# Kernel tuning notes

Hardware: AMD Instinct MI355X
Metric: run time of the kernel (lower is better)

The kernel has to match this reference:

```python
import jax, jax.numpy as jnp
import numpy as np

B = 256      # number of graphs (args.batch_size)
NPG = 1000   # nodes per graph (args.num_node)
C = 64       # in_channels
DEG = 16     # avg degree
K = 500      # ceil(ratio * NPG), ratio = 0.5
EPS = 1e-8


def setup_inputs() -> dict:
    key = jax.random.key(0)
    k1, k2, k3, k4, k5 = jax.random.split(key, 5)
    N = B * NPG
    epg = NPG * DEG  # edges per graph
    x = jax.random.normal(k1, (N, C), jnp.float32)
    src = jax.random.randint(k2, (B, epg), 0, NPG)
    dst = jax.random.randint(k3, (B, epg), 0, NPG)
    off = (jnp.arange(B, dtype=jnp.int32) * NPG)[:, None]
    edge_index = jnp.stack([(src + off).reshape(-1), (dst + off).reshape(-1)]).astype(jnp.int32)
    edge_attr = jax.random.uniform(k4, (B * epg,), jnp.float32)
    batch = jnp.repeat(jnp.arange(B, dtype=jnp.int32), NPG)
    W = jax.random.normal(k5, (C, C), jnp.float32) * (1.0 / np.sqrt(C))
    b = jnp.zeros((C,), jnp.float32)
    return {"istraining": 1, "x": x, "edge_index": edge_index, "edge_attr": edge_attr,
            "batch": batch, "W": W, "b": b}


def _gcn_conv(x, edge_index, W, b):
    # PyG GCNConv: x' = D^{-1/2} (A + I) D^{-1/2} X W + b, unit edge weights.
    N = x.shape[0]
    sl = jnp.arange(N, dtype=edge_index.dtype)
    src = jnp.concatenate([edge_index[0], sl])  # message source j
    dst = jnp.concatenate([edge_index[1], sl])  # aggregation target i
    deg = jnp.zeros((N,), x.dtype).at[dst].add(1.0)
    dinv = jnp.where(deg > 0, jax.lax.rsqrt(jnp.maximum(deg, 1.0)), 0.0)
    norm = dinv[src] * dinv[dst]          # [E+N]
    h = x @ W                              # [N, C]
    msg = h[src] * norm[:, None]           # gather + scale (dominant traffic)
    out = jax.ops.segment_sum(msg, dst, num_segments=N) + b
    return out


def _node_score(x):
    # compute_node_score: cosine similarity of each node to its graph centroid
    # (community prototype), plus KL(softmax(score) || uniform) per graph.
    xb = x.reshape(B, NPG, C)
    cen = xb.mean(axis=1, keepdims=True)                       # [B,1,C]
    num = jnp.sum(xb * cen, axis=-1)                           # [B,NPG]
    den = jnp.linalg.norm(xb, axis=-1) * jnp.linalg.norm(cen, axis=-1) + EPS
    score = num / den                                          # [B,NPG]
    logp = jax.nn.log_softmax(score, axis=1)
    kl = jnp.sum(jnp.exp(logp) * (logp + jnp.log(jnp.float32(NPG))), axis=1)  # [B]
    indices_ = jnp.argsort(-score, axis=1)                     # [B,NPG]
    return score, kl, indices_


def reference(istraining, x, edge_index, edge_attr, batch, W, b):
    N = x.shape[0]
    x = _gcn_conv(x, edge_index, W, b)
    score, kl_all_batch, indices_ = _node_score(x)
    # per-graph top-k (fixed k since every graph has NPG nodes)
    _, idx = jax.lax.top_k(score, K)                           # [B,K]
    perm = ((jnp.arange(B, dtype=idx.dtype) * NPG)[:, None] + idx).reshape(-1)  # [B*K]
    score_flat = score.reshape(-1)
    x_new = x[perm] * jnp.tanh(score_flat[perm])[:, None]
    batch_new = batch[perm]
    # filter_adj: keep edges with both endpoints retained, re-index to new ids.
    mapping = jnp.full((N,), -1, dtype=jnp.int32).at[perm].set(
        jnp.arange(perm.shape[0], dtype=jnp.int32))
    new_ei = mapping[edge_index]                               # [2,E], -1 = dropped
    edge_mask = jnp.logical_and(new_ei[0] >= 0, new_ei[1] >= 0)
    edge_attr_new = jnp.where(edge_mask, edge_attr, 0.0)
    return (x_new, new_ei, edge_attr_new, edge_mask, batch_new, perm, kl_all_batch, indices_)
```

## Files before the change

kernel.cpp:

```cpp
#include <hip/hip_runtime.h>
#include <math.h>

#define NPG 1000
#define KTOP 500
#define C 64
#define EPG 16000

__device__ __forceinline__ float readlane_f(float v, int l) {
    return __uint_as_float(__builtin_amdgcn_readlane(__float_as_uint(v), (unsigned)l));
}
__device__ __forceinline__ int readlane_i(int v, int l) {
    return (int)__builtin_amdgcn_readlane((unsigned)v, (unsigned)l);
}

__global__ __launch_bounds__(256) void build_graph_k(const int* __restrict__ ei, int E,
                                                     int* __restrict__ deg,
                                                     float* __restrict__ dinv,
                                                     int* __restrict__ off,
                                                     int* __restrict__ csr,
                                                     float* __restrict__ wcsr) {
    int g = blockIdx.x, t = threadIdx.x;
    __shared__ int cnt[NPG];
    __shared__ int soff[NPG];
    __shared__ float sdinv[NPG];
    __shared__ unsigned short lcsr[EPG];
    __shared__ int red[256];
    const int gbase = g * NPG;
    const int ebase = g * EPG;
    const int* __restrict__ srcp = ei + ebase;
    const int* __restrict__ dstp = ei + E + ebase;

    for (int i = t; i < NPG; i += 256) cnt[i] = 0;
    __syncthreads();
    for (int i = t; i < EPG; i += 256) atomicAdd(&cnt[dstp[i] - gbase], 1);
    __syncthreads();
    int base = t * 4;
    int v0 = 0, v1 = 0, v2 = 0, v3 = 0;
    if (base + 0 < NPG) v0 = cnt[base + 0];
    if (base + 1 < NPG) v1 = cnt[base + 1];
    if (base + 2 < NPG) v2 = cnt[base + 2];
    if (base + 3 < NPG) v3 = cnt[base + 3];
    int s = v0 + v1 + v2 + v3;
    red[t] = s;
    __syncthreads();
    for (int o = 1; o < 256; o <<= 1) {
        int xx = (t >= o) ? red[t - o] : 0;
        __syncthreads();
        red[t] += xx;
        __syncthreads();
    }
    int p = red[t] - s;
    if (base + 0 < NPG) { soff[base + 0] = p; p += v0; }
    if (base + 1 < NPG) { soff[base + 1] = p; p += v1; }
    if (base + 2 < NPG) { soff[base + 2] = p; p += v2; }
    if (base + 3 < NPG) { soff[base + 3] = p; p += v3; }
    __syncthreads();
    for (int i = t; i < NPG; i += 256) {
        int d = cnt[i];
        deg[gbase + i] = d;
        float dv = 1.0f / sqrtf((float)(d + 1));
        dinv[gbase + i] = dv;
        sdinv[i] = dv;
        off[gbase + i] = ebase + soff[i];
    }
    __syncthreads();
    for (int i = t; i < NPG; i += 256) cnt[i] = soff[i];
    __syncthreads();
    for (int i = t; i < EPG; i += 256) {
        int d = dstp[i] - gbase;
        int pos = atomicAdd(&cnt[d], 1);
        lcsr[pos] = (unsigned short)(srcp[i] - gbase);
    }
    __syncthreads();
    int4* co = (int4*)(csr + ebase);
    float4* wo = (float4*)(wcsr + ebase);
    for (int i = t; i < EPG / 4; i += 256) {
        int l0 = lcsr[i * 4 + 0], l1 = lcsr[i * 4 + 1];
        int l2 = lcsr[i * 4 + 2], l3 = lcsr[i * 4 + 3];
        int4 v;
        v.x = gbase + l0; v.y = gbase + l1; v.z = gbase + l2; v.w = gbase + l3;
        co[i] = v;
        float4 w;
        w.x = sdinv[l0]; w.y = sdinv[l1]; w.z = sdinv[l2]; w.w = sdinv[l3];
        wo[i] = w;
    }
}

__global__ __launch_bounds__(256) void gemm_k(const float* __restrict__ x,
                                              const float* __restrict__ W,
                                              float* __restrict__ h, int N) {
    __shared__ float sW[C * C];
    int t = threadIdx.x;
    for (int i = t; i < C * C / 4; i += 256) ((float4*)sW)[i] = ((const float4*)W)[i];
    __syncthreads();
    int r0 = blockIdx.x * 512 + t;
    int r1 = r0 + 256;
    if (r0 >= N) return;
    bool has1 = (r1 < N);
    const float4* x0 = (const float4*)(x + (size_t)r0 * C);
    const float4* x1 = (const float4*)(x + (size_t)(has1 ? r1 : r0) * C);
    float acc0[C], acc1[C];
#pragma unroll
    for (int i = 0; i < C; ++i) { acc0[i] = 0.f; acc1[i] = 0.f; }
    float4 a0 = x0[0], a1 = x1[0];
    for (int k4 = 0; k4 < 16; ++k4) {
        float4 b0, b1;
        if (k4 < 15) { b0 = x0[k4 + 1]; b1 = x1[k4 + 1]; }
        const float4* wr = (const float4*)(sW + k4 * 4 * C);
        const float* a0f = (const float*)&a0;
        const float* a1f = (const float*)&a1;
#pragma unroll
        for (int c4 = 0; c4 < 16; ++c4) {
            float4 w[4];
            w[0] = wr[c4]; w[1] = wr[16 + c4]; w[2] = wr[32 + c4]; w[3] = wr[48 + c4];
            const float* wf = (const float*)w;
#pragma unroll
            for (int j = 0; j < 4; ++j) {
                float s0 = acc0[c4 * 4 + j], s1 = acc1[c4 * 4 + j];
#pragma unroll
                for (int kk = 0; kk < 4; ++kk) {
                    float wv = wf[kk * 4 + j];
                    s0 = fmaf(a0f[kk], wv, s0);
                    s1 = fmaf(a1f[kk], wv, s1);
                }
                acc0[c4 * 4 + j] = s0; acc1[c4 * 4 + j] = s1;
            }
        }
        a0 = b0; a1 = b1;
    }
    float4* h0 = (float4*)(h + (size_t)r0 * C);
#pragma unroll
    for (int q = 0; q < 16; ++q) h0[q] = ((float4*)acc0)[q];
    if (has1) {
        float4* h1 = (float4*)(h + (size_t)r1 * C);
#pragma unroll
        for (int q = 0; q < 16; ++q) h1[q] = ((float4*)acc1)[q];
    }
}

__global__ __launch_bounds__(256) void gather_k(const int* __restrict__ csr,
                                                const float* __restrict__ wcsr,
                                                const int* __restrict__ off,
                                                const int* __restrict__ deg,
                                                const float* __restrict__ h,
                                                const float* __restrict__ dinv,
                                                const float* __restrict__ bias,
                                                float* __restrict__ out2, int N, int B) {
    int b = blockIdx.x;
    int wave = threadIdx.x >> 6;
    int lane = threadIdx.x & 63;
    int node;
    if ((B & 7) == 0) {
        int xcd = b & 7, slot = b >> 3;
        int gpx = B >> 3;
        int g = xcd * gpx + slot / (NPG / 4);
        int blkin = slot % (NPG / 4);
        node = g * NPG + blkin * 4 + wave;
    } else {
        node = b * 4 + wave;
    }
    if (node >= N) return;
    int o0 = off[node], dg = deg[node];
    float di = dinv[node];
    float hv = h[(size_t)node * C + lane];
    int sv = 0; float wv = 0.f;
    if (lane < dg) { sv = csr[o0 + lane]; wv = wcsr[o0 + lane]; }
    float acc = 0.f;
    int jmax = dg < 64 ? dg : 64;
    int j = 0;
    for (; j + 4 <= jmax; j += 4) {
        int   s0 = readlane_i(sv, j + 0); float w0 = readlane_f(wv, j + 0);
        int   s1 = readlane_i(sv, j + 1); float w1 = readlane_f(wv, j + 1);
        int   s2 = readlane_i(sv, j + 2); float w2 = readlane_f(wv, j + 2);
        int   s3 = readlane_i(sv, j + 3); float w3 = readlane_f(wv, j + 3);
        float h0 = h[(size_t)s0 * C + lane];
        float h1 = h[(size_t)s1 * C + lane];
        float h2 = h[(size_t)s2 * C + lane];
        float h3 = h[(size_t)s3 * C + lane];
        acc = fmaf(h0, w0, acc);
        acc = fmaf(h1, w1, acc);
        acc = fmaf(h2, w2, acc);
        acc = fmaf(h3, w3, acc);
    }
    for (; j < jmax; ++j) {
        int s = readlane_i(sv, j); float w = readlane_f(wv, j);
        acc = fmaf(h[(size_t)s * C + lane], w, acc);
    }
    for (; j < dg; ++j) {
        int s = csr[o0 + j];
        acc = fmaf(h[(size_t)s * C + lane], dinv[s], acc);
    }
    out2[(size_t)node * C + lane] = bias[lane] + di * acc + di * di * hv;
}

__global__ void centroid_part_k(const float* __restrict__ out2, float* __restrict__ pcen) {
    int blk = blockIdx.x;
    int g = blk >> 2, p = blk & 3;
    int t = threadIdx.x;
    int c = t & 63, q = t >> 6;
    const float* base = out2 + (size_t)g * NPG * C;
    int n0 = p * 250, n1 = n0 + 250;
    float acc = 0.f;
    for (int n = n0 + q; n < n1; n += 4) acc += base[(size_t)n * C + c];
    __shared__ float red[256];
    red[t] = acc;
    __syncthreads();
    if (t < 64) pcen[(size_t)blk * C + t] = red[t] + red[64 + t] + red[128 + t] + red[192 + t];
}

__global__ void cen_fin_k(const float* __restrict__ pcen, float* __restrict__ cen,
                          float* __restrict__ cnorm) {
    int g = blockIdx.x, c = threadIdx.x;
    float s = pcen[(size_t)(g * 4 + 0) * C + c] + pcen[(size_t)(g * 4 + 1) * C + c]
            + pcen[(size_t)(g * 4 + 2) * C + c] + pcen[(size_t)(g * 4 + 3) * C + c];
    float m = s / 1000.0f;
    cen[g * C + c] = m;
    float v = m * m;
    for (int o = 32; o > 0; o >>= 1) v += __shfl_down(v, o, 64);
    if (c == 0) cnorm[g] = sqrtf(v);
}

__global__ void score_k(const float* __restrict__ out2, const float* __restrict__ cen,
                        const float* __restrict__ cnorm, float* __restrict__ score, int N) {
    int i = blockIdx.x * 256 + threadIdx.x;
    if (i < N) {
        int g = i / NPG;
        const float4* xr = (const float4*)(out2 + (size_t)i * C);
        const float4* cr = (const float4*)(cen + g * C);
        float num = 0.f, sq = 0.f;
#pragma unroll
        for (int q = 0; q < 16; ++q) {
            float4 a = xr[q], b = cr[q];
            num += a.x * b.x + a.y * b.y + a.z * b.z + a.w * b.w;
            sq  += a.x * a.x + a.y * a.y + a.z * a.z + a.w * a.w;
        }
        float den = sqrtf(sq) * cnorm[g] + 1e-8f;
        score[i] = num / den;
    }
}

__global__ void softmax_kl_k(const float* __restrict__ score, float* __restrict__ o_kl) {
    int g = blockIdx.x, t = threadIdx.x;
    __shared__ float ss[NPG];
    __shared__ float red[256];
    const float4* s4 = (const float4*)(score + (size_t)g * NPG);
    for (int i = t; i < NPG / 4; i += 256) ((float4*)ss)[i] = s4[i];
    __syncthreads();
    float mx = -INFINITY;
    for (int i = t; i < NPG; i += 256) mx = fmaxf(mx, ss[i]);
    red[t] = mx;
    __syncthreads();
    for (int w = 128; w > 0; w >>= 1) { if (t < w) red[t] = fmaxf(red[t], red[t + w]); __syncthreads(); }
    mx = red[0];
    __syncthreads();
    float se = 0.f;
    for (int i = t; i < NPG; i += 256) se += expf(ss[i] - mx);
    red[t] = se;
    __syncthreads();
    for (int w = 128; w > 0; w >>= 1) { if (t < w) red[t] += red[t + w]; __syncthreads(); }
    float lse = logf(red[0]);
    __syncthreads();
    float kl = 0.f;
    const float ln_npg = 6.9077552790f;
    for (int i = t; i < NPG; i += 256) {
        float lp = ss[i] - mx - lse;
        kl += expf(lp) * (lp + ln_npg);
    }
    red[t] = kl;
    __syncthreads();
    for (int w = 128; w > 0; w >>= 1) { if (t < w) red[t] += red[t + w]; __syncthreads(); }
    if (t == 0) o_kl[g] = red[0];
}

__global__ void sort_k(const float* __restrict__ score, int* __restrict__ sidx,
                       float* __restrict__ o_ind) {
    __shared__ unsigned long long kk[1024];
    int g = blockIdx.x, t = threadIdx.x;
    for (int i = t; i < 1024; i += 512) {
        unsigned long long v;
        if (i < NPG) {
            unsigned u = __float_as_uint(score[(size_t)g * NPG + i]);
            u = (u & 0x80000000u) ? ~u : (u | 0x80000000u);
            v = ((unsigned long long)(~u) << 32) | (unsigned)i;
        } else {
            v = ~0ULL;
        }
        kk[i] = v;
    }
    __syncthreads();
    for (int k = 2; k <= 1024; k <<= 1) {
        for (int j = k >> 1; j > 0; j >>= 1) {
            for (int i = t; i < 1024; i += 512) {
                int ixj = i ^ j;
                if (ixj > i) {
                    unsigned long long a = kk[i], b = kk[ixj];
                    bool up = ((i & k) == 0);
                    if ((a > b) == up) { kk[i] = b; kk[ixj] = a; }
                }
            }
            __syncthreads();
        }
    }
    for (int i = t; i < NPG; i += 512) {
        int idx = (int)(kk[i] & 0xFFFFFFFFULL);
        sidx[(size_t)g * NPG + i] = idx;
        o_ind[(size_t)g * NPG + i] = (float)idx;
    }
}

__global__ void topk_k(const int* __restrict__ sidx, const float* __restrict__ score,
                       const float* __restrict__ out2, int* __restrict__ mapping,
                       float* __restrict__ o_xnew, float* __restrict__ o_batch,
                       float* __restrict__ o_perm, int BK) {
    int j = blockIdx.x * 256 + threadIdx.x;
    if (j < BK) {
        int b = j / KTOP, r = j - b * KTOP;
        int node = sidx[(size_t)b * NPG + r];
        int gn = b * NPG + node;
        mapping[gn] = j;
        o_perm[j] = (float)gn;
        o_batch[j] = (float)b;
        float tn = tanhf(score[gn]);
        const float4* src = (const float4*)(out2 + (size_t)gn * C);
        float4* dst = (float4*)(o_xnew + (size_t)j * C);
#pragma unroll
        for (int q = 0; q < 16; ++q) {
            float4 v = src[q];
            v.x *= tn; v.y *= tn; v.z *= tn; v.w *= tn;
            dst[q] = v;
        }
    }
}

__global__ void edge_out_k(const int* __restrict__ ei, const float* __restrict__ eattr,
                           const int* __restrict__ mapping, float* __restrict__ o_newei,
                           float* __restrict__ o_eattr, float* __restrict__ o_mask, int E) {
    int e4 = blockIdx.x * 256 + threadIdx.x;
    int q = E >> 2;
    if (e4 < q) {
        int4 sidx = ((const int4*)ei)[e4];
        int4 didx = ((const int4*)ei)[q + e4];
        int a0 = mapping[sidx.x], a1 = mapping[sidx.y], a2 = mapping[sidx.z], a3 = mapping[sidx.w];
        int b0 = mapping[didx.x], b1 = mapping[didx.y], b2 = mapping[didx.z], b3 = mapping[didx.w];
        float4 f0 = { (float)a0, (float)a1, (float)a2, (float)a3 };
        float4 f1 = { (float)b0, (float)b1, (float)b2, (float)b3 };
        ((float4*)o_newei)[e4] = f0;
        ((float4*)o_newei)[q + e4] = f1;
        float4 at = ((const float4*)eattr)[e4];
        float4 mk, ea;
        mk.x = (a0 >= 0 && b0 >= 0) ? 1.0f : 0.0f;
        mk.y = (a1 >= 0 && b1 >= 0) ? 1.0f : 0.0f;
        mk.z = (a2 >= 0 && b2 >= 0) ? 1.0f : 0.0f;
        mk.w = (a3 >= 0 && b3 >= 0) ? 1.0f : 0.0f;
        ea.x = mk.x != 0.0f ? at.x : 0.0f;
        ea.y = mk.y != 0.0f ? at.y : 0.0f;
        ea.z = mk.z != 0.0f ? at.z : 0.0f;
        ea.w = mk.w != 0.0f ? at.w : 0.0f;
        ((float4*)o_mask)[e4] = mk;
        ((float4*)o_eattr)[e4] = ea;
    }
}

extern "C" void kernel_launch(void* const* d_in, const int* in_sizes, int n_in,
                              void* d_out, int out_size, void* d_ws, size_t ws_size,
                              hipStream_t stream) {
    (void)n_in; (void)out_size; (void)ws_size;
    const float* x     = (const float*)d_in[1];
    const int*   ei    = (const int*)d_in[2];
    const float* eattr = (const float*)d_in[3];
    const float* W     = (const float*)d_in[5];
    const float* bias  = (const float*)d_in[6];

    const int N  = in_sizes[1] / C;
    const int E  = in_sizes[2] / 2;
    const int B  = N / NPG;
    const int BK = B * KTOP;

    char* wsp = (char*)d_ws;
    float* out2    = (float*)wsp; wsp += (size_t)N * C * 4;
    float* dinv    = (float*)wsp; wsp += (size_t)N * 4;
    float* score   = (float*)wsp; wsp += (size_t)N * 4;
    float* cen     = (float*)wsp; wsp += (size_t)B * C * 4;
    float* cnorm   = (float*)wsp; wsp += 1024;
    int*   sidx    = (int*)wsp;   wsp += (size_t)B * NPG * 4;
    int*   mapping = (int*)wsp;   wsp += (size_t)N * 4;
    int*   deg     = (int*)wsp;   wsp += (size_t)N * 4;
    int*   off     = (int*)wsp;   wsp += (size_t)N * 4;
    float* pcen    = (float*)wsp; wsp += (size_t)B * 4 * C * 4;

    float* out     = (float*)d_out;
    float* o_xnew  = out;
    float* o_newei = o_xnew + (size_t)BK * C;
    float* o_eattr = o_newei + 2 * (size_t)E;
    float* o_mask  = o_eattr + (size_t)E;
    float* o_batch = o_mask + (size_t)E;
    float* o_perm  = o_batch + (size_t)BK;
    float* o_kl    = o_perm + (size_t)BK;
    float* o_ind   = o_kl + (size_t)B;

    float* hbuf = out;
    int*   csr  = (int*)o_eattr;
    float* wcsr = o_mask;

    hipMemsetAsync(mapping, 0xFF, (size_t)N * 4, stream);

    build_graph_k<<<B, 256, 0, stream>>>(ei, E, deg, dinv, off, csr, wcsr);
    gemm_k<<<(N + 511) / 512, 256, 0, stream>>>(x, W, hbuf, N);
    gather_k<<<(N + 3) / 4, 256, 0, stream>>>(csr, wcsr, off, deg, hbuf, dinv, bias, out2, N, B);
    centroid_part_k<<<B * 4, 256, 0, stream>>>(out2, pcen);
    cen_fin_k<<<B, 64, 0, stream>>>(pcen, cen, cnorm);
    score_k<<<(N + 255) / 256, 256, 0, stream>>>(out2, cen, cnorm, score, N);
    softmax_kl_k<<<B, 256, 0, stream>>>(score, o_kl);
    sort_k<<<B, 512, 0, stream>>>(score, sidx, o_ind);
    topk_k<<<(BK + 255) / 256, 256, 0, stream>>>(sidx, score, out2, mapping,
                                                 o_xnew, o_batch, o_perm, BK);
    edge_out_k<<<(E / 4 + 255) / 256, 256, 0, stream>>>(ei, eattr, mapping,
                                                        o_newei, o_eattr, o_mask, E);
}
```

Measured before the change: 494.8 us.

## Prescale GEMM output by source dinv and drop per-edge weight array

Folds the source-side D^{-1/2} normalization into the GEMM epilogue, so h2 = dinv*xW is stored directly. The gather then only sums neighbor rows, and the per-edge weight array (wcsr) no longer has to be built, written or read, which removes one global write and one read per edge along with the readlane ops. The gather inner loop is also unrolled to 8 neighbors to put more loads in flight. The GEMM gains a dependency on dinv, and the floating-point summation order changes slightly.

Result: no change. 491.7 us (-0.6%).

```diff
diff --git a/kernel.cpp b/kernel.cpp
--- a/kernel.cpp
+++ b/kernel.cpp
@@ -17,12 +17,10 @@
                                                      int* __restrict__ deg,
                                                      float* __restrict__ dinv,
                                                      int* __restrict__ off,
-                                                     int* __restrict__ csr,
-                                                     float* __restrict__ wcsr) {
+                                                     int* __restrict__ csr) {
     int g = blockIdx.x, t = threadIdx.x;
     __shared__ int cnt[NPG];
     __shared__ int soff[NPG];
-    __shared__ float sdinv[NPG];
     __shared__ unsigned short lcsr[EPG];
     __shared__ int red[256];
     const int gbase = g * NPG;
@@ -58,9 +56,7 @@
     for (int i = t; i < NPG; i += 256) {
         int d = cnt[i];
         deg[gbase + i] = d;
-        float dv = 1.0f / sqrtf((float)(d + 1));
-        dinv[gbase + i] = dv;
-        sdinv[i] = dv;
+        dinv[gbase + i] = 1.0f / sqrtf((float)(d + 1));
         off[gbase + i] = ebase + soff[i];
     }
     __syncthreads();
@@ -73,22 +69,20 @@
     }
     __syncthreads();
     int4* co = (int4*)(csr + ebase);
-    float4* wo = (float4*)(wcsr + ebase);
     for (int i = t; i < EPG / 4; i += 256) {
-        int l0 = lcsr[i * 4 + 0], l1 = lcsr[i * 4 + 1];
-        int l2 = lcsr[i * 4 + 2], l3 = lcsr[i * 4 + 3];
         int4 v;
-        v.x = gbase + l0; v.y = gbase + l1; v.z = gbase + l2; v.w = gbase + l3;
+        v.x = gbase + (int)lcsr[i * 4 + 0];
+        v.y = gbase + (int)lcsr[i * 4 + 1];
+        v.z = gbase + (int)lcsr[i * 4 + 2];
+        v.w = gbase + (int)lcsr[i * 4 + 3];
         co[i] = v;
-        float4 w;
-        w.x = sdinv[l0]; w.y = sdinv[l1]; w.z = sdinv[l2]; w.w = sdinv[l3];
-        wo[i] = w;
     }
 }
 
 __global__ __launch_bounds__(256) void gemm_k(const float* __restrict__ x,
                                               const float* __restrict__ W,
-                                              float* __restrict__ h, int N) {
+                                              const float* __restrict__ dinv,
+                                              float* __restrict__ h2, int N) {
     __shared__ float sW[C * C];
     int t = threadIdx.x;
     for (int i = t; i < C * C / 4; i += 256) ((float4*)sW)[i] = ((const float4*)W)[i];
@@ -128,21 +122,24 @@
         }
         a0 = b0; a1 = b1;
     }
-    float4* h0 = (float4*)(h + (size_t)r0 * C);
+    float dv0 = dinv[r0];
+    float dv1 = has1 ? dinv[r1] : 0.f;
+#pragma unroll
+    for (int i = 0; i < C; ++i) { acc0[i] *= dv0; acc1[i] *= dv1; }
+    float4* h0 = (float4*)(h2 + (size_t)r0 * C);
 #pragma unroll
     for (int q = 0; q < 16; ++q) h0[q] = ((float4*)acc0)[q];
     if (has1) {
-        float4* h1 = (float4*)(h + (size_t)r1 * C);
+        float4* h1 = (float4*)(h2 + (size_t)r1 * C);
 #pragma unroll
         for (int q = 0; q < 16; ++q) h1[q] = ((float4*)acc1)[q];
     }
 }
 
 __global__ __launch_bounds__(256) void gather_k(const int* __restrict__ csr,
-                                                const float* __restrict__ wcsr,
                                                 const int* __restrict__ off,
                                                 const int* __restrict__ deg,
-                                                const float* __restrict__ h,
+                                                const float* __restrict__ h2,
                                                 const float* __restrict__ dinv,
                                                 const float* __restrict__ bias,
                                                 float* __restrict__ out2, int N, int B) {
@@ -162,35 +159,51 @@
     if (node >= N) return;
     int o0 = off[node], dg = deg[node];
     float di = dinv[node];
-    float hv = h[(size_t)node * C + lane];
-    int sv = 0; float wv = 0.f;
-    if (lane < dg) { sv = csr[o0 + lane]; wv = wcsr[o0 + lane]; }
+    float hv2 = h2[(size_t)node * C + lane];
+    int sv = 0;
+    if (lane < dg) sv = csr[o0 + lane];
     float acc = 0.f;
     int jmax = dg < 64 ? dg : 64;
     int j = 0;
+    for (; j + 8 <= jmax; j += 8) {
+        int s0 = readlane_i(sv, j + 0);
+        int s1 = readlane_i(sv, j + 1);
+        int s2 = readlane_i(sv, j + 2);
+        int s3 = readlane_i(sv, j + 3);
+        int s4 = readlane_i(sv, j + 4);
+        int s5 = readlane_i(sv, j + 5);
+        int s6 = readlane_i(sv, j + 6);
+        int s7 = readlane_i(sv, j + 7);
+        float v0 = h2[(size_t)s0 * C + lane];
+        float v1 = h2[(size_t)s1 * C + lane];
+        float v2 = h2[(size_t)s2 * C + lane];
+        float v3 = h2[(size_t)s3 * C + lane];
+        float v4 = h2[(size_t)s4 * C + lane];
+        float v5 = h2[(size_t)s5 * C + lane];
+        float v6 = h2[(size_t)s6 * C + lane];
+        float v7 = h2[(size_t)s7 * C + lane];
+        acc += ((v0 + v1) + (v2 + v3)) + ((v4 + v5) + (v6 + v7));
+    }
     for (; j + 4 <= jmax; j += 4) {
-        int   s0 = readlane_i(sv, j + 0); float w0 = readlane_f(wv, j + 0);
-        int   s1 = readlane_i(sv, j + 1); float w1 = readlane_f(wv, j + 1);
-        int   s2 = readlane_i(sv, j + 2); float w2 = readlane_f(wv, j + 2);
-        int   s3 = readlane_i(sv, j + 3); float w3 = readlane_f(wv, j + 3);
-        float h0 = h[(size_t)s0 * C + lane];
-        float h1 = h[(size_t)s1 * C + lane];
-        float h2 = h[(size_t)s2 * C + lane];
-        float h3 = h[(size_t)s3 * C + lane];
-        acc = fmaf(h0, w0, acc);
-        acc = fmaf(h1, w1, acc);
-        acc = fmaf(h2, w2, acc);
-        acc = fmaf(h3, w3, acc);
+        int s0 = readlane_i(sv, j + 0);
+        int s1 = readlane_i(sv, j + 1);
+        int s2 = readlane_i(sv, j + 2);
+        int s3 = readlane_i(sv, j + 3);
+        float v0 = h2[(size_t)s0 * C + lane];
+        float v1 = h2[(size_t)s1 * C + lane];
+        float v2 = h2[(size_t)s2 * C + lane];
+        float v3 = h2[(size_t)s3 * C + lane];
+        acc += (v0 + v1) + (v2 + v3);
     }
     for (; j < jmax; ++j) {
-        int s = readlane_i(sv, j); float w = readlane_f(wv, j);
-        acc = fmaf(h[(size_t)s * C + lane], w, acc);
+        int s = readlane_i(sv, j);
+        acc += h2[(size_t)s * C + lane];
     }
     for (; j < dg; ++j) {
         int s = csr[o0 + j];
-        acc = fmaf(h[(size_t)s * C + lane], dinv[s], acc);
-    }
-    out2[(size_t)node * C + lane] = bias[lane] + di * acc + di * di * hv;
+        acc += h2[(size_t)s * C + lane];
+    }
+    out2[(size_t)node * C + lane] = bias[lane] + di * (acc + hv2);
 }
 
 __global__ void centroid_part_k(const float* __restrict__ out2, float* __restrict__ pcen) {
@@ -398,15 +411,14 @@
     float* o_kl    = o_perm + (size_t)BK;
     float* o_ind   = o_kl + (size_t)B;
 
-    float* hbuf = out;
-    int*   csr  = (int*)o_eattr;
-    float* wcsr = o_mask;
+    float* h2buf = out;
+    int*   csr   = (int*)o_eattr;
 
     hipMemsetAsync(mapping, 0xFF, (size_t)N * 4, stream);
 
-    build_graph_k<<<B, 256, 0, stream>>>(ei, E, deg, dinv, off, csr, wcsr);
-    gemm_k<<<(N + 511) / 512, 256, 0, stream>>>(x, W, hbuf, N);
-    gather_k<<<(N + 3) / 4, 256, 0, stream>>>(csr, wcsr, off, deg, hbuf, dinv, bias, out2, N, B);
+    build_graph_k<<<B, 256, 0, stream>>>(ei, E, deg, dinv, off, csr);
+    gemm_k<<<(N + 511) / 512, 256, 0, stream>>>(x, W, dinv, h2buf, N);
+    gather_k<<<(N + 3) / 4, 256, 0, stream>>>(csr, off, deg, h2buf, dinv, bias, out2, N, B);
     centroid_part_k<<<B * 4, 256, 0, stream>>>(out2, pcen);
     cen_fin_k<<<B, 64, 0, stream>>>(pcen, cen, cnorm);
     score_k<<<(N + 255) / 256, 256, 0, stream>>>(out2, cen, cnorm, score, N);
```
